# Kernel optimization log

Measured on AMD Instinct MI355X. Metric: run time of the kernel, lower is better.

## Reference

```python
import jax, jax.numpy as jnp
import numpy as np

B, N, E = 64, 512, 262144
D_EMB = 128   # 2 * embedding_dim
D_H = 128     # residue_emb_dim == iegmn_lay_hid_dim
L = 5         # iegmn_n_lays
X_INIT = 0.25 # residual mix toward original coords (IEGMN x_connection_init)


def silu(x):
    return x * jax.nn.sigmoid(x)


def _edges(k):
    # within-graph random edges: pick a graph, then a node inside it
    g = jax.random.randint(k, (E,), 0, B)
    n = jax.random.randint(jax.random.fold_in(k, 1), (E,), 0, N)
    return (g * N + n).astype(jnp.int32)


def setup_inputs() -> dict:
    key = jax.random.key(0)
    ks = jax.random.split(key, 16)
    Nt = B * N
    s = 0.05
    feat = jax.random.normal(ks[0], (Nt, D_EMB), jnp.float32)
    coords = jax.random.normal(ks[1], (Nt, 3), jnp.float32)
    c_valid = (jax.random.uniform(ks[2], (B, N)) > 0.3).astype(jnp.float32)
    c_valid = c_valid.at[:, 0].set(1.0)  # avoid empty graphs
    return {
        'feat': feat,
        'coords': coords,
        'c_valid': c_valid,
        'edge_src': _edges(ks[3]), 'edge_dst': _edges(ks[4]),
        'cross_src': _edges(ks[5]), 'cross_dst': _edges(ks[6]),
        'W_emb': jax.random.normal(ks[7], (D_H, D_EMB), jnp.float32) * s,
        'We1': jax.random.normal(ks[8], (L, 2 * D_H + 1, D_H), jnp.float32) * s,
        'be1': jnp.zeros((L, D_H), jnp.float32),
        'We2': jax.random.normal(ks[9], (L, D_H, D_H), jnp.float32) * s,
        'be2': jnp.zeros((L, D_H), jnp.float32),
        'Wx': jax.random.normal(ks[10], (L, D_H, 1), jnp.float32) * s,
        'Wh': jax.random.normal(ks[11], (L, 3 * D_H, D_H), jnp.float32) * s,
        'bh': jnp.zeros((L, D_H), jnp.float32),
        'Wfc': jax.random.normal(ks[12], (3, D_H, D_H), jnp.float32) * s,
        'bfc': jnp.zeros((3, D_H), jnp.float32),
        'Wout': jax.random.normal(ks[13], (D_H, 1), jnp.float32) * s,
        'bout': jnp.zeros((1,), jnp.float32),
    }


def _deg_inv(dst, n):
    deg = jax.ops.segment_sum(jnp.ones(dst.shape[0], jnp.float32), dst, num_segments=n)
    return (1.0 / jnp.maximum(deg, 1.0))[:, None]


def _iegmn_layer(p, src, dst, x, h, x0, h0, deg_inv):
    We1, be1, We2, be2, Wx, Wh, bh = p
    n = x.shape[0]
    dx = x[src] - x[dst]                                  # [E, 3]
    d2 = jnp.sum(dx * dx, -1, keepdims=True)              # [E, 1]
    m = silu(jnp.concatenate([h[src], h[dst], d2], -1) @ We1 + be1)
    m = silu(m @ We2 + be2)                               # [E, D_H]
    coef = jnp.tanh(m @ Wx)                               # [E, 1]
    agg_x = jax.ops.segment_sum(dx * coef, dst, num_segments=n) * deg_inv
    x_new = X_INIT * x0 + (1.0 - X_INIT) * x + agg_x
    agg_m = jax.ops.segment_sum(m, dst, num_segments=n) * deg_inv
    h_new = silu(jnp.concatenate([h, agg_m, h0], -1) @ Wh + bh)
    return x_new, h_new


def reference(feat, coords, c_valid, edge_src, edge_dst, cross_src, cross_dst,
              W_emb, We1, be1, We2, be2, Wx, Wh, bh, Wfc, bfc, Wout, bout):
    Nt = feat.shape[0]
    h = feat @ W_emb.T          # embede (no bias)
    h0, x0, x = h, coords, coords
    dgi = _deg_inv(edge_dst, Nt)
    dci = _deg_inv(cross_dst, Nt)
    for k in range(L):
        p = tuple(t[k] for t in (We1, be1, We2, be2, Wx, Wh, bh))
        # branch == 'both': run layer on graph then cross_graph with same input h
        x, c1 = _iegmn_layer(p, edge_src, edge_dst, x, h, x0, h0, dgi)
        x, c2 = _iegmn_layer(p, cross_src, cross_dst, x, h, x0, h0, dci)
        h = c2 - c1             # dropout is identity at inference
    # masked sum-pool / count
    hb = h.reshape(B, N, D_H)
    pooled = jnp.sum(hb * c_valid[..., None], axis=1) / jnp.sum(c_valid, axis=1, keepdims=True)
    z = pooled
    for i in range(Wfc.shape[0]):
        z = jax.nn.relu(z @ Wfc[i] + bfc[i])
    out = jax.nn.sigmoid(z @ Wout + bout)
    return out.reshape(-1)      # [B]
```

## Files before the change

### kernel.cpp

```cpp
#include <hip/hip_runtime.h>

#define DEVINL __device__ __forceinline__

constexpr int NT   = 32768;
constexpr int DH   = 128;
constexpr int NE   = 262144;
constexpr int BGR  = 64;
constexpr int NPG  = 512;
constexpr int LAYS = 5;

typedef __attribute__((ext_vector_type(8))) short bf16x8;
typedef __attribute__((ext_vector_type(4))) float f32x4;
typedef __attribute__((ext_vector_type(4))) unsigned int uint4v;
typedef unsigned int uint;

DEVINL float siluf(float v){ return v * (1.0f/(1.0f + __expf(-v))); }

DEVINL uint bf16_rne(float f){
  uint x = __float_as_uint(f);
  return (x + 0x7fffu + ((x>>16)&1u)) >> 16;
}

DEVINL void split8(const float* m, bf16x8& h, bf16x8& l){
  #pragma unroll
  for (int j=0;j<8;j++){
    uint x  = __float_as_uint(m[j]);
    uint hb = x >> 16;
    float hf = __uint_as_float(hb<<16);
    uint lb = bf16_rne(m[j] - hf);
    h[j] = (short)hb; l[j] = (short)lb;
  }
}

DEVINL f32x4 mma3(const uint* __restrict__ w, int i0, int i1,
                  bf16x8 ah, bf16x8 al, f32x4 acc){
  uint4v u0 = *(const uint4v*)(w + i0);
  uint4v u1 = *(const uint4v*)(w + i1);
  bf16x8 bh, bl;
  #pragma unroll
  for (int j=0;j<4;j++){
    bh[j]   = (short)(u0[j]>>16); bl[j]   = (short)(u0[j]&0xffffu);
    bh[j+4] = (short)(u1[j]>>16); bl[j+4] = (short)(u1[j]&0xffffu);
  }
  acc = __builtin_amdgcn_mfma_f32_16x16x32_bf16(al, bh, acc, 0,0,0);
  acc = __builtin_amdgcn_mfma_f32_16x16x32_bf16(ah, bl, acc, 0,0,0);
  acc = __builtin_amdgcn_mfma_f32_16x16x32_bf16(ah, bh, acc, 0,0,0);
  return acc;
}

template<int TRANS>
__global__ __launch_bounds__(256) void k_prep(const float* __restrict__ src, uint* __restrict__ dst){
  const int idx = blockIdx.x*256 + threadIdx.x;
  const int k = idx>>7, col = idx&127;
  const float v = TRANS ? src[(size_t)col*128 + k] : src[(size_t)k*128 + col];
  uint hb = __float_as_uint(v) >> 16;
  float hf = __uint_as_float(hb<<16);
  uint lb = bf16_rne(v - hf);
  const int kc = k>>5, kin = k&31, s = kin>>2;
  dst[kc*4096 + col*32 + (((s ^ (col&7)))<<2) + (kin&3)] = (hb<<16) | lb;
}

__global__ __launch_bounds__(256) void k_hist(const int* __restrict__ dst, int* __restrict__ cnt){
  int e = blockIdx.x*256 + threadIdx.x;
  atomicAdd(&cnt[dst[e]], 1);
}

__global__ __launch_bounds__(1024) void k_scan(const int* __restrict__ cnt, int* __restrict__ cur){
  __shared__ int part[1024];
  const int tid = threadIdx.x;
  const int base = tid*32;
  int s = 0;
  for (int i=0;i<32;i++) s += cnt[base+i];
  const int own = s;
  part[tid] = s; __syncthreads();
  for (int off=1; off<1024; off<<=1){
    int v = (tid>=off) ? part[tid-off] : 0;
    __syncthreads();
    part[tid] += v;
    __syncthreads();
  }
  int run = part[tid] - own;
  for (int i=0;i<32;i++){ cur[base+i] = run; run += cnt[base+i]; }
}

__global__ __launch_bounds__(256) void k_invdeg(const int* __restrict__ cnt, float* __restrict__ dinv){
  int n = blockIdx.x*256 + threadIdx.x;
  int c = cnt[n];
  dinv[n] = 1.0f / (float)(c > 1 ? c : 1);
}

__global__ __launch_bounds__(256) void k_scatter(const int* __restrict__ dst, int* __restrict__ cur,
                                                 int* __restrict__ perm){
  int e = blockIdx.x*256 + threadIdx.x;
  int p = atomicAdd(&cur[dst[e]], 1);
  perm[p] = e;
}

template<int MODE>
__global__ __launch_bounds__(512) void k_ngemm(
    const float* __restrict__ A0, const float* __restrict__ A1, const float* __restrict__ A2,
    const float* __restrict__ dinv, const uint* __restrict__ W0, const uint* __restrict__ W1,
    const float* __restrict__ bias, const float* __restrict__ c1in,
    float* __restrict__ out0, float* __restrict__ out1)
{
  __shared__ __align__(16) uint wbuf[8192];
  const int tid = threadIdx.x;
  const int wv = tid>>6, lane = tid&63, c = lane&15, q = lane>>4;
  const int row = blockIdx.x*128 + wv*16 + c;
  float dv = 1.0f;
  if constexpr (MODE>=2) dv = dinv[row];
  f32x4 accA[8], accB[8];
  #pragma unroll
  for (int t=0;t<8;t++){
    #pragma unroll
    for (int r=0;r<4;r++){ accA[t][r]=0.f; if constexpr (MODE==1) accB[t][r]=0.f; }
  }
  const int swz0 = (((2*q)  ^(c&7))<<2);
  const int swz1 = (((2*q+1)^(c&7))<<2);
  constexpr int NST = (MODE==1) ? 4 : ((MODE>=2) ? 6 : 2);
  for (int st=0; st<NST; ++st){
    __syncthreads();
    if constexpr (MODE==1){
      #pragma unroll
      for (int i=0;i<2;i++){
        ((uint4v*)wbuf)[tid + i*512]        = ((const uint4v*)(W0 + st*4096))[tid + i*512];
        ((uint4v*)(wbuf+4096))[tid + i*512] = ((const uint4v*)(W1 + st*4096))[tid + i*512];
      }
    } else {
      #pragma unroll
      for (int i=0;i<4;i++)
        ((uint4v*)wbuf)[tid + i*512] = ((const uint4v*)(W0 + st*8192))[tid + i*512];
    }
    __syncthreads();
    if constexpr (MODE==1){
      const int kb = st*32 + q*8;
      float4 v0 = *(const float4*)(A0 + (size_t)row*128 + kb);
      float4 v1 = *(const float4*)(A0 + (size_t)row*128 + kb + 4);
      float m[8] = {v0.x,v0.y,v0.z,v0.w,v1.x,v1.y,v1.z,v1.w};
      bf16x8 ah, al; split8(m, ah, al);
      #pragma unroll
      for (int t=0;t<8;t++){
        const int base = t*512 + c*32;
        accA[t] = mma3(wbuf,      base+swz0, base+swz1, ah, al, accA[t]);
        accB[t] = mma3(wbuf+4096, base+swz0, base+swz1, ah, al, accB[t]);
      }
    } else {
      #pragma unroll
      for (int ks=0; ks<2; ++ks){
        const int kc = st*2 + ks;
        const float* asrc = A0; float sc = 1.0f;
        if constexpr (MODE>=2){
          if (kc >= 8)      { asrc = A2; }
          else if (kc >= 4) { asrc = A1; sc = dv; }
        }
        const int koff = (kc&3)*32 + q*8;
        float4 v0 = *(const float4*)(asrc + (size_t)row*128 + koff);
        float4 v1 = *(const float4*)(asrc + (size_t)row*128 + koff + 4);
        float m[8] = {v0.x*sc,v0.y*sc,v0.z*sc,v0.w*sc,v1.x*sc,v1.y*sc,v1.z*sc,v1.w*sc};
        bf16x8 ah, al; split8(m, ah, al);
        #pragma unroll
        for (int t=0;t<8;t++){
          const int base = ks*4096 + t*512 + c*32;
          accA[t] = mma3(wbuf, base+swz0, base+swz1, ah, al, accA[t]);
        }
      }
    }
  }
  #pragma unroll
  for (int t=0;t<8;t++){
    const int col = t*16 + c;
    float b0 = 0.f;
    if constexpr (MODE!=0) b0 = bias[col];
    #pragma unroll
    for (int r=0;r<4;r++){
      const size_t orow = (size_t)blockIdx.x*128 + wv*16 + q*4 + r;
      float v = accA[t][r];
      if constexpr (MODE==0){
        out0[orow*128 + col] = v; out1[orow*128 + col] = v;
      } else if constexpr (MODE==1){
        out0[orow*128 + col] = v + b0;
        out1[orow*128 + col] = accB[t][r];
      } else if constexpr (MODE==2){
        out0[orow*128 + col] = siluf(v + b0);
      } else {
        out0[orow*128 + col] = siluf(v + b0) - c1in[orow*128 + col];
      }
    }
  }
}

__global__ __launch_bounds__(512) void k_edge(
    const int* __restrict__ perm, const int* __restrict__ esrc, const int* __restrict__ edst,
    const float* __restrict__ x,  const float* __restrict__ Aw, const float* __restrict__ Bw,
    const uint* __restrict__ w2p, const float* __restrict__ We1_l,
    const float* __restrict__ be2_l, const float* __restrict__ Wx_l,
    float* __restrict__ aggm, float* __restrict__ aggx)
{
  __shared__ __align__(16) uint  w2t[8192];
  __shared__ __align__(16) float w256s[128];
  __shared__ __align__(16) float wxs[128];
  __shared__ __align__(16) float be2s[128];
  __shared__ float dxs[128][3];
  __shared__ int   dsts[128];
  const int tid = threadIdx.x;
  const int wv = tid>>6, lane = tid&63, c = lane&15, q = lane>>4;
  if (tid < 128){ w256s[tid]=We1_l[256*128+tid]; wxs[tid]=Wx_l[tid]; be2s[tid]=be2_l[tid]; }
  const int er = wv*16 + c;
  const int eg = perm[blockIdx.x*128 + er];
  const int s  = esrc[eg], d = edst[eg];
  const float dx0 = x[s*3+0]-x[d*3+0];
  const float dx1 = x[s*3+1]-x[d*3+1];
  const float dx2 = x[s*3+2]-x[d*3+2];
  const float d2  = dx0*dx0 + dx1*dx1 + dx2*dx2;
  if (lane < 16){ dxs[er][0]=dx0; dxs[er][1]=dx1; dxs[er][2]=dx2; dsts[er]=d; }
  f32x4 acc[8];
  #pragma unroll
  for (int t=0;t<8;t++){ acc[t][0]=0.f; acc[t][1]=0.f; acc[t][2]=0.f; acc[t][3]=0.f; }
  const int swz0 = (((2*q)  ^(c&7))<<2);
  const int swz1 = (((2*q+1)^(c&7))<<2);
  const float* ap = Aw + (size_t)s*128;
  const float* bp = Bw + (size_t)d*128;
  for (int half=0; half<2; ++half){
    __syncthreads();
    #pragma unroll
    for (int i=0;i<4;i++)
      ((uint4v*)w2t)[tid + i*512] = ((const uint4v*)(w2p + half*8192))[tid + i*512];
    __syncthreads();
    #pragma unroll
    for (int ks=0; ks<2; ++ks){
      const int kb = half*64 + ks*32 + q*8;
      float4 av0 = *(const float4*)(ap+kb), av1 = *(const float4*)(ap+kb+4);
      float4 bv0 = *(const float4*)(bp+kb), bv1 = *(const float4*)(bp+kb+4);
      float4 w0  = *(const float4*)&w256s[kb], w1 = *(const float4*)&w256s[kb+4];
      float m[8];
      m[0]=siluf(av0.x+bv0.x+d2*w0.x); m[1]=siluf(av0.y+bv0.y+d2*w0.y);
      m[2]=siluf(av0.z+bv0.z+d2*w0.z); m[3]=siluf(av0.w+bv0.w+d2*w0.w);
      m[4]=siluf(av1.x+bv1.x+d2*w1.x); m[5]=siluf(av1.y+bv1.y+d2*w1.y);
      m[6]=siluf(av1.z+bv1.z+d2*w1.z); m[7]=siluf(av1.w+bv1.w+d2*w1.w);
      bf16x8 ah, al; split8(m, ah, al);
      #pragma unroll
      for (int t=0;t<8;t++){
        const int base = ks*4096 + t*512 + c*32;
        acc[t] = mma3(w2t, base+swz0, base+swz1, ah, al, acc[t]);
      }
    }
  }
  float pd[4];
  #pragma unroll
  for (int t=0;t<8;t++){
    const float be = be2s[t*16+c], wx = wxs[t*16+c];
    #pragma unroll
    for (int r=0;r<4;r++){
      float v = siluf(acc[t][r] + be);
      acc[t][r] = v;
      if (t==0) pd[r] = v*wx; else pd[r] += v*wx;
    }
  }
  #pragma unroll
  for (int msk=1; msk<16; msk<<=1){
    #pragma unroll
    for (int r=0;r<4;r++) pd[r] += __shfl_xor(pd[r], msk);
  }
  float coef[4];
  #pragma unroll
  for (int r=0;r<4;r++) coef[r] = tanhf(pd[r]);
  const int r0 = wv*16 + q*4;
  {
    int i = 0;
    while (i < 4){
      const int dd = dsts[r0+i];
      float sv[8];
      #pragma unroll
      for (int t=0;t<8;t++) sv[t] = acc[t][i];
      int i2 = i+1;
      while (i2 < 4 && dsts[r0+i2] == dd){
        #pragma unroll
        for (int t=0;t<8;t++) sv[t] += acc[t][i2];
        ++i2;
      }
      float* bm = aggm + (size_t)dd*128 + c;
      #pragma unroll
      for (int t=0;t<8;t++) unsafeAtomicAdd(bm + t*16, sv[t]);
      i = i2;
    }
  }
  if (c < 3){
    int i = 0;
    while (i < 4){
      const int dd = dsts[r0+i];
      float sv = dxs[r0+i][c]*coef[i];
      int i2 = i+1;
      while (i2 < 4 && dsts[r0+i2] == dd){ sv += dxs[r0+i2][c]*coef[i2]; ++i2; }
      unsafeAtomicAdd(aggx + (size_t)dd*3 + c, sv);
      i = i2;
    }
  }
}

__global__ __launch_bounds__(256) void k_xupd(float* __restrict__ x, const float* __restrict__ x0,
                                              const float* __restrict__ aggx,
                                              const float* __restrict__ dinv){
  int i = blockIdx.x*256 + threadIdx.x;
  if (i < NT*3){
    int n = i/3;
    x[i] = 0.25f*x0[i] + 0.75f*x[i] + aggx[i]*dinv[n];
  }
}

__global__ __launch_bounds__(128) void k_pool(const float* __restrict__ h,
                                              const float* __restrict__ cvalid,
                                              float* __restrict__ pooled){
  const int b = blockIdx.x, j = threadIdx.x;
  float s = 0.f, cf = 0.f;
  for (int n=0;n<NPG;n++){
    const float m = cvalid[b*NPG + n];
    s  += h[((size_t)b*NPG + n)*DH + j] * m;
    cf += m;
  }
  pooled[b*DH + j] = s / cf;
}

__global__ __launch_bounds__(256) void k_mlp(const float* __restrict__ pooled,
                                             const float* __restrict__ Wfc,
                                             const float* __restrict__ bfc,
                                             const float* __restrict__ Wout,
                                             const float* __restrict__ bout,
                                             float* __restrict__ out)
{
  __shared__ __align__(16) float z[64*132];
  __shared__ __align__(16) float wB[128*128];
  const int t = threadIdx.x;
  {
    const int n = t>>2, qq = t&3;
    const float4* p = (const float4*)(pooled + n*DH + qq*32);
    float4* w = (float4*)&z[n*132 + qq*32];
    #pragma unroll
    for (int u=0;u<8;u++) w[u] = p[u];
  }
  const int g = t>>5, lane = t&31, c0 = lane*4;
  for (int l=0;l<3;l++){
    #pragma unroll
    for (int i=0;i<16;i++){
      const int idx = t + i*256;
      ((float4*)wB)[idx] = ((const float4*)(Wfc + (size_t)l*DH*DH))[idx];
    }
    __syncthreads();
    float acc[8][4];
    #pragma unroll
    for (int i=0;i<8;i++){ acc[i][0]=0.f; acc[i][1]=0.f; acc[i][2]=0.f; acc[i][3]=0.f; }
    #pragma unroll 4
    for (int kk=0; kk<128; kk+=4){
      float4 b0=*(const float4*)&wB[(kk+0)*128+c0];
      float4 b1=*(const float4*)&wB[(kk+1)*128+c0];
      float4 b2=*(const float4*)&wB[(kk+2)*128+c0];
      float4 b3=*(const float4*)&wB[(kk+3)*128+c0];
      #pragma unroll
      for (int i=0;i<8;i++){
        float4 a=*(const float4*)&z[(g*8+i)*132 + kk];
        acc[i][0]+=a.x*b0.x+a.y*b1.x+a.z*b2.x+a.w*b3.x;
        acc[i][1]+=a.x*b0.y+a.y*b1.y+a.z*b2.y+a.w*b3.y;
        acc[i][2]+=a.x*b0.z+a.y*b1.z+a.z*b2.z+a.w*b3.z;
        acc[i][3]+=a.x*b0.w+a.y*b1.w+a.z*b2.w+a.w*b3.w;
      }
    }
    __syncthreads();
    #pragma unroll
    for (int i=0;i<8;i++){
      float v0=acc[i][0]+bfc[l*DH+c0+0]; v0 = v0>0.f?v0:0.f;
      float v1=acc[i][1]+bfc[l*DH+c0+1]; v1 = v1>0.f?v1:0.f;
      float v2=acc[i][2]+bfc[l*DH+c0+2]; v2 = v2>0.f?v2:0.f;
      float v3=acc[i][3]+bfc[l*DH+c0+3]; v3 = v3>0.f?v3:0.f;
      float4 v; v.x=v0; v.y=v1; v.z=v2; v.w=v3;
      *(float4*)&z[(g*8+i)*132 + c0] = v;
    }
    __syncthreads();
  }
  if (t < 64){
    float a = 0.f;
    for (int k2=0;k2<128;k2++) a += z[t*132 + k2]*Wout[k2];
    out[t] = 1.0f/(1.0f + __expf(-(a + bout[0])));
  }
}

extern "C" void kernel_launch(void* const* d_in, const int* in_sizes, int n_in,
                              void* d_out, int out_size, void* d_ws, size_t ws_size,
                              hipStream_t stream)
{
  (void)in_sizes; (void)n_in; (void)out_size; (void)ws_size;
  const float* feat   = (const float*)d_in[0];
  const float* coords = (const float*)d_in[1];
  const float* cvalid = (const float*)d_in[2];
  const int*   esrc   = (const int*)d_in[3];
  const int*   edst   = (const int*)d_in[4];
  const int*   csrc   = (const int*)d_in[5];
  const int*   cdst   = (const int*)d_in[6];
  const float* W_emb  = (const float*)d_in[7];
  const float* We1    = (const float*)d_in[8];
  const float* be1    = (const float*)d_in[9];
  const float* We2    = (const float*)d_in[10];
  const float* be2    = (const float*)d_in[11];
  const float* Wx     = (const float*)d_in[12];
  const float* Wh     = (const float*)d_in[13];
  const float* bh     = (const float*)d_in[14];
  const float* Wfc    = (const float*)d_in[15];
  const float* bfc    = (const float*)d_in[16];
  const float* Wout   = (const float*)d_in[17];
  const float* bout   = (const float*)d_in[18];

  float* ws = (float*)d_ws;
  float* h      = ws; ws += (size_t)NT*DH;
  float* h0     = ws; ws += (size_t)NT*DH;
  float* c1     = ws; ws += (size_t)NT*DH;
  float* Aw     = ws; ws += (size_t)NT*DH;
  float* Bw     = ws; ws += (size_t)NT*DH;
  float* aggm   = ws; ws += (size_t)NT*DH;
  float* x      = ws; ws += (size_t)NT*3;
  float* aggx   = ws; ws += (size_t)NT*3;
  float* dgi    = ws; ws += NT;
  float* dci    = ws; ws += NT;
  float* pooled = ws; ws += BGR*DH;
  int* permG  = (int*)ws; ws += NE;
  int* permC  = (int*)ws; ws += NE;
  int* cnt    = (int*)ws; ws += NT;
  int* cursor = (int*)ws; ws += NT;
  uint* pst    = (uint*)ws;
  uint* wemb_p = pst;
  const size_t LSTR = 16384*3 + 49152;
  uint* lay_p  = pst + 16384;

  k_prep<1><<<64, 256, 0, stream>>>(W_emb, wemb_p);
  for (int k=0;k<LAYS;k++){
    uint* p = lay_p + (size_t)k*LSTR;
    k_prep<0><<<64,  256, 0, stream>>>(We1 + (size_t)k*257*DH,            p);
    k_prep<0><<<64,  256, 0, stream>>>(We1 + (size_t)k*257*DH + 128*DH,   p + 16384);
    k_prep<0><<<64,  256, 0, stream>>>(We2 + (size_t)k*DH*DH,             p + 32768);
    k_prep<0><<<192, 256, 0, stream>>>(Wh  + (size_t)k*3*DH*DH,           p + 49152);
  }

  hipMemsetAsync(cnt, 0, NT*sizeof(int), stream);
  k_hist   <<<NE/256, 256, 0, stream>>>(edst, cnt);
  k_scan   <<<1, 1024, 0, stream>>>(cnt, cursor);
  k_invdeg <<<NT/256, 256, 0, stream>>>(cnt, dgi);
  k_scatter<<<NE/256, 256, 0, stream>>>(edst, cursor, permG);
  hipMemsetAsync(cnt, 0, NT*sizeof(int), stream);
  k_hist   <<<NE/256, 256, 0, stream>>>(cdst, cnt);
  k_scan   <<<1, 1024, 0, stream>>>(cnt, cursor);
  k_invdeg <<<NT/256, 256, 0, stream>>>(cnt, dci);
  k_scatter<<<NE/256, 256, 0, stream>>>(cdst, cursor, permC);

  k_ngemm<0><<<NT/128, 512, 0, stream>>>(feat, nullptr, nullptr, nullptr,
                                         wemb_p, nullptr, nullptr, nullptr, h, h0);
  hipMemcpyAsync(x, coords, (size_t)NT*3*sizeof(float), hipMemcpyDeviceToDevice, stream);

  for (int k=0; k<LAYS; k++){
    uint* p = lay_p + (size_t)k*LSTR;
    const float* We1_l = We1 + (size_t)k*257*DH;
    const float* be1_l = be1 + (size_t)k*DH;
    const float* be2_l = be2 + (size_t)k*DH;
    const float* Wx_l  = Wx  + (size_t)k*DH;
    const float* bh_l  = bh  + (size_t)k*DH;

    k_ngemm<1><<<NT/128, 512, 0, stream>>>(h, nullptr, nullptr, nullptr,
                                           p, p + 16384, be1_l, nullptr, Aw, Bw);
    hipMemsetAsync(aggm, 0, (size_t)NT*DH*sizeof(float), stream);
    hipMemsetAsync(aggx, 0, (size_t)NT*3*sizeof(float), stream);
    k_edge<<<NE/128, 512, 0, stream>>>(permG, esrc, edst, x, Aw, Bw,
                                       p + 32768, We1_l, be2_l, Wx_l, aggm, aggx);
    k_xupd<<<(NT*3+255)/256, 256, 0, stream>>>(x, coords, aggx, dgi);
    k_ngemm<2><<<NT/128, 512, 0, stream>>>(h, aggm, h0, dgi,
                                           p + 49152, nullptr, bh_l, nullptr, c1, nullptr);
    hipMemsetAsync(aggm, 0, (size_t)NT*DH*sizeof(float), stream);
    hipMemsetAsync(aggx, 0, (size_t)NT*3*sizeof(float), stream);
    k_edge<<<NE/128, 512, 0, stream>>>(permC, csrc, cdst, x, Aw, Bw,
                                       p + 32768, We1_l, be2_l, Wx_l, aggm, aggx);
    k_xupd<<<(NT*3+255)/256, 256, 0, stream>>>(x, coords, aggx, dci);
    k_ngemm<3><<<NT/128, 512, 0, stream>>>(h, aggm, h0, dci,
                                           p + 49152, nullptr, bh_l, c1, h, nullptr);
  }

  k_pool<<<BGR, 128, 0, stream>>>(h, cvalid, pooled);
  k_mlp <<<1, 256, 0, stream>>>(pooled, Wfc, bfc, Wout, bout, (float*)d_out);
}
```

Measured before the change: 1.875 ms.

## Pre-split bf16 weight layout, fuse agg zeroing into consumers, fast tanh, parallel pool

Stores weights pre-split into separate hi/lo bf16 planes so MFMA B operands load directly from LDS without per-use unpacking. Removes the per-layer memsets by zeroing aggm inside the node GEMM after it reads it and aggx inside the x update. Also swaps tanhf for an exp-based approximation and spreads the pooling reduction over 512 threads. The in-kernel zeroing adds extra global writes, and the fast tanh may overflow or lose accuracy for large inputs.

```diff
diff --git a/kernel.cpp b/kernel.cpp
--- a/kernel.cpp
+++ b/kernel.cpp
@@ -15,6 +15,7 @@
 typedef unsigned int uint;
 
 DEVINL float siluf(float v){ return v * (1.0f/(1.0f + __expf(-v))); }
+DEVINL float tanh_fast(float x){ float e = __expf(2.0f*x); return 1.0f - 2.0f/(e + 1.0f); }
 
 DEVINL uint bf16_rne(float f){
   uint x = __float_as_uint(f);
@@ -32,16 +33,7 @@
   }
 }
 
-DEVINL f32x4 mma3(const uint* __restrict__ w, int i0, int i1,
-                  bf16x8 ah, bf16x8 al, f32x4 acc){
-  uint4v u0 = *(const uint4v*)(w + i0);
-  uint4v u1 = *(const uint4v*)(w + i1);
-  bf16x8 bh, bl;
-  #pragma unroll
-  for (int j=0;j<4;j++){
-    bh[j]   = (short)(u0[j]>>16); bl[j]   = (short)(u0[j]&0xffffu);
-    bh[j+4] = (short)(u1[j]>>16); bl[j+4] = (short)(u1[j]&0xffffu);
-  }
+DEVINL f32x4 mma3(bf16x8 ah, bf16x8 al, bf16x8 bh, bf16x8 bl, f32x4 acc){
   acc = __builtin_amdgcn_mfma_f32_16x16x32_bf16(al, bh, acc, 0,0,0);
   acc = __builtin_amdgcn_mfma_f32_16x16x32_bf16(ah, bl, acc, 0,0,0);
   acc = __builtin_amdgcn_mfma_f32_16x16x32_bf16(ah, bh, acc, 0,0,0);
@@ -49,15 +41,17 @@
 }
 
 template<int TRANS>
-__global__ __launch_bounds__(256) void k_prep(const float* __restrict__ src, uint* __restrict__ dst){
+__global__ __launch_bounds__(256) void k_prep(const float* __restrict__ src, short* __restrict__ dst){
   const int idx = blockIdx.x*256 + threadIdx.x;
   const int k = idx>>7, col = idx&127;
   const float v = TRANS ? src[(size_t)col*128 + k] : src[(size_t)k*128 + col];
   uint hb = __float_as_uint(v) >> 16;
   float hf = __uint_as_float(hb<<16);
   uint lb = bf16_rne(v - hf);
-  const int kc = k>>5, kin = k&31, s = kin>>2;
-  dst[kc*4096 + col*32 + (((s ^ (col&7)))<<2) + (kin&3)] = (hb<<16) | lb;
+  const int kc = k>>5, q = (k&31)>>3, j = k&7;
+  const size_t o = (size_t)kc*8192 + q*1024 + col*8 + j;
+  dst[o]        = (short)hb;
+  dst[o + 4096] = (short)lb;
 }
 
 __global__ __launch_bounds__(256) void k_hist(const int* __restrict__ dst, int* __restrict__ cnt){
@@ -98,12 +92,12 @@
 
 template<int MODE>
 __global__ __launch_bounds__(512) void k_ngemm(
-    const float* __restrict__ A0, const float* __restrict__ A1, const float* __restrict__ A2,
-    const float* __restrict__ dinv, const uint* __restrict__ W0, const uint* __restrict__ W1,
+    const float* __restrict__ A0, float* __restrict__ A1, const float* __restrict__ A2,
+    const float* __restrict__ dinv, const short* __restrict__ W0, const short* __restrict__ W1,
     const float* __restrict__ bias, const float* __restrict__ c1in,
     float* __restrict__ out0, float* __restrict__ out1)
 {
-  __shared__ __align__(16) uint wbuf[8192];
+  __shared__ __align__(16) short wbuf[16384];
   const int tid = threadIdx.x;
   const int wv = tid>>6, lane = tid&63, c = lane&15, q = lane>>4;
   const int row = blockIdx.x*128 + wv*16 + c;
@@ -115,21 +109,20 @@
     #pragma unroll
     for (int r=0;r<4;r++){ accA[t][r]=0.f; if constexpr (MODE==1) accB[t][r]=0.f; }
   }
-  const int swz0 = (((2*q)  ^(c&7))<<2);
-  const int swz1 = (((2*q+1)^(c&7))<<2);
+  const int fo = q*1024 + c*8;
   constexpr int NST = (MODE==1) ? 4 : ((MODE>=2) ? 6 : 2);
   for (int st=0; st<NST; ++st){
     __syncthreads();
     if constexpr (MODE==1){
       #pragma unroll
       for (int i=0;i<2;i++){
-        ((uint4v*)wbuf)[tid + i*512]        = ((const uint4v*)(W0 + st*4096))[tid + i*512];
-        ((uint4v*)(wbuf+4096))[tid + i*512] = ((const uint4v*)(W1 + st*4096))[tid + i*512];
+        ((uint4v*)wbuf)[tid + i*512]         = ((const uint4v*)(W0 + st*8192))[tid + i*512];
+        ((uint4v*)(wbuf+8192))[tid + i*512]  = ((const uint4v*)(W1 + st*8192))[tid + i*512];
       }
     } else {
       #pragma unroll
       for (int i=0;i<4;i++)
-        ((uint4v*)wbuf)[tid + i*512] = ((const uint4v*)(W0 + st*8192))[tid + i*512];
+        ((uint4v*)wbuf)[tid + i*512] = ((const uint4v*)(W0 + (size_t)st*16384))[tid + i*512];
     }
     __syncthreads();
     if constexpr (MODE==1){
@@ -140,28 +133,39 @@
       bf16x8 ah, al; split8(m, ah, al);
       #pragma unroll
       for (int t=0;t<8;t++){
-        const int base = t*512 + c*32;
-        accA[t] = mma3(wbuf,      base+swz0, base+swz1, ah, al, accA[t]);
-        accB[t] = mma3(wbuf+4096, base+swz0, base+swz1, ah, al, accB[t]);
+        bf16x8 bhA = *(const bf16x8*)&wbuf[t*128 + fo];
+        bf16x8 blA = *(const bf16x8*)&wbuf[4096 + t*128 + fo];
+        bf16x8 bhB = *(const bf16x8*)&wbuf[8192 + t*128 + fo];
+        bf16x8 blB = *(const bf16x8*)&wbuf[12288 + t*128 + fo];
+        accA[t] = mma3(ah, al, bhA, blA, accA[t]);
+        accB[t] = mma3(ah, al, bhB, blB, accB[t]);
       }
     } else {
       #pragma unroll
       for (int ks=0; ks<2; ++ks){
         const int kc = st*2 + ks;
-        const float* asrc = A0; float sc = 1.0f;
+        const float* asrc = A0; float sc = 1.0f; bool zero_a1 = false;
         if constexpr (MODE>=2){
           if (kc >= 8)      { asrc = A2; }
-          else if (kc >= 4) { asrc = A1; sc = dv; }
+          else if (kc >= 4) { asrc = A1; sc = dv; zero_a1 = true; }
         }
         const int koff = (kc&3)*32 + q*8;
         float4 v0 = *(const float4*)(asrc + (size_t)row*128 + koff);
         float4 v1 = *(const float4*)(asrc + (size_t)row*128 + koff + 4);
+        if constexpr (MODE>=2){
+          if (zero_a1){
+            float4 z; z.x=0.f; z.y=0.f; z.z=0.f; z.w=0.f;
+            *(float4*)(A1 + (size_t)row*128 + koff)     = z;
+            *(float4*)(A1 + (size_t)row*128 + koff + 4) = z;
+          }
+        }
         float m[8] = {v0.x*sc,v0.y*sc,v0.z*sc,v0.w*sc,v1.x*sc,v1.y*sc,v1.z*sc,v1.w*sc};
         bf16x8 ah, al; split8(m, ah, al);
         #pragma unroll
         for (int t=0;t<8;t++){
-          const int base = ks*4096 + t*512 + c*32;
-          accA[t] = mma3(wbuf, base+swz0, base+swz1, ah, al, accA[t]);
+          bf16x8 bh = *(const bf16x8*)&wbuf[ks*8192 + t*128 + fo];
+          bf16x8 bl = *(const bf16x8*)&wbuf[ks*8192 + 4096 + t*128 + fo];
+          accA[t] = mma3(ah, al, bh, bl, accA[t]);
         }
       }
     }
@@ -192,11 +196,11 @@
 __global__ __launch_bounds__(512) void k_edge(
     const int* __restrict__ perm, const int* __restrict__ esrc, const int* __restrict__ edst,
     const float* __restrict__ x,  const float* __restrict__ Aw, const float* __restrict__ Bw,
-    const uint* __restrict__ w2p, const float* __restrict__ We1_l,
+    const short* __restrict__ w2p, const float* __restrict__ We1_l,
     const float* __restrict__ be2_l, const float* __restrict__ Wx_l,
     float* __restrict__ aggm, float* __restrict__ aggx)
 {
-  __shared__ __align__(16) uint  w2t[8192];
+  __shared__ __align__(16) short w2t[16384];
   __shared__ __align__(16) float w256s[128];
   __shared__ __align__(16) float wxs[128];
   __shared__ __align__(16) float be2s[128];
@@ -216,15 +220,14 @@
   f32x4 acc[8];
   #pragma unroll
   for (int t=0;t<8;t++){ acc[t][0]=0.f; acc[t][1]=0.f; acc[t][2]=0.f; acc[t][3]=0.f; }
-  const int swz0 = (((2*q)  ^(c&7))<<2);
-  const int swz1 = (((2*q+1)^(c&7))<<2);
+  const int fo = q*1024 + c*8;
   const float* ap = Aw + (size_t)s*128;
   const float* bp = Bw + (size_t)d*128;
   for (int half=0; half<2; ++half){
     __syncthreads();
     #pragma unroll
     for (int i=0;i<4;i++)
-      ((uint4v*)w2t)[tid + i*512] = ((const uint4v*)(w2p + half*8192))[tid + i*512];
+      ((uint4v*)w2t)[tid + i*512] = ((const uint4v*)(w2p + half*16384))[tid + i*512];
     __syncthreads();
     #pragma unroll
     for (int ks=0; ks<2; ++ks){
@@ -240,8 +243,9 @@
       bf16x8 ah, al; split8(m, ah, al);
       #pragma unroll
       for (int t=0;t<8;t++){
-        const int base = ks*4096 + t*512 + c*32;
-        acc[t] = mma3(w2t, base+swz0, base+swz1, ah, al, acc[t]);
+        bf16x8 bh = *(const bf16x8*)&w2t[ks*8192 + t*128 + fo];
+        bf16x8 bl = *(const bf16x8*)&w2t[ks*8192 + 4096 + t*128 + fo];
+        acc[t] = mma3(ah, al, bh, bl, acc[t]);
       }
     }
   }
@@ -263,7 +267,7 @@
   }
   float coef[4];
   #pragma unroll
-  for (int r=0;r<4;r++) coef[r] = tanhf(pd[r]);
+  for (int r=0;r<4;r++) coef[r] = tanh_fast(pd[r]);
   const int r0 = wv*16 + q*4;
   {
     int i = 0;
@@ -298,26 +302,36 @@
 }
 
 __global__ __launch_bounds__(256) void k_xupd(float* __restrict__ x, const float* __restrict__ x0,
-                                              const float* __restrict__ aggx,
+                                              float* __restrict__ aggx,
                                               const float* __restrict__ dinv){
   int i = blockIdx.x*256 + threadIdx.x;
   if (i < NT*3){
     int n = i/3;
     x[i] = 0.25f*x0[i] + 0.75f*x[i] + aggx[i]*dinv[n];
-  }
-}
-
-__global__ __launch_bounds__(128) void k_pool(const float* __restrict__ h,
+    aggx[i] = 0.f;
+  }
+}
+
+__global__ __launch_bounds__(512) void k_pool(const float* __restrict__ h,
                                               const float* __restrict__ cvalid,
                                               float* __restrict__ pooled){
-  const int b = blockIdx.x, j = threadIdx.x;
+  __shared__ float red[4][128];
+  __shared__ float redc[4];
+  const int b = blockIdx.x, t = threadIdx.x, j = t&127, sl = t>>7;
   float s = 0.f, cf = 0.f;
-  for (int n=0;n<NPG;n++){
+  for (int n=sl; n<NPG; n+=4){
     const float m = cvalid[b*NPG + n];
     s  += h[((size_t)b*NPG + n)*DH + j] * m;
     cf += m;
   }
-  pooled[b*DH + j] = s / cf;
+  red[sl][j] = s;
+  if (j==0) redc[sl] = cf;
+  __syncthreads();
+  if (t < 128){
+    float ss = red[0][t]+red[1][t]+red[2][t]+red[3][t];
+    float cc = redc[0]+redc[1]+redc[2]+redc[3];
+    pooled[b*DH + t] = ss / cc;
+  }
 }
 
 __global__ __launch_bounds__(256) void k_mlp(const float* __restrict__ pooled,
@@ -423,18 +437,21 @@
   int* permC  = (int*)ws; ws += NE;
   int* cnt    = (int*)ws; ws += NT;
   int* cursor = (int*)ws; ws += NT;
-  uint* pst    = (uint*)ws;
-  uint* wemb_p = pst;
-  const size_t LSTR = 16384*3 + 49152;
-  uint* lay_p  = pst + 16384;
+  short* pst    = (short*)ws;
+  short* wemb_p = pst;
+  const size_t LSTR = 32768*3 + 98304;
+  short* lay_p  = pst + 32768;
+
+  hipMemsetAsync(aggm, 0, (size_t)NT*DH*sizeof(float), stream);
+  hipMemsetAsync(aggx, 0, (size_t)NT*3*sizeof(float), stream);
 
   k_prep<1><<<64, 256, 0, stream>>>(W_emb, wemb_p);
   for (int k=0;k<LAYS;k++){
-    uint* p = lay_p + (size_t)k*LSTR;
-    k_prep<0><<<64,  256, 0, stream>>>(We1 + (size_t)k*257*DH,            p);
-    k_prep<0><<<64,  256, 0, stream>>>(We1 + (size_t)k*257*DH + 128*DH,   p + 16384);
-    k_prep<0><<<64,  256, 0, stream>>>(We2 + (size_t)k*DH*DH,             p + 32768);
-    k_prep<0><<<192, 256, 0, stream>>>(Wh  + (size_t)k*3*DH*DH,           p + 49152);
+    short* p = lay_p + (size_t)k*LSTR;
+    k_prep<0><<<64,  256, 0, stream>>>(We1 + (size_t)k*257*DH,          p);
+    k_prep<0><<<64,  256, 0, stream>>>(We1 + (size_t)k*257*DH + 128*DH, p + 32768);
+    k_prep<0><<<64,  256, 0, stream>>>(We2 + (size_t)k*DH*DH,           p + 65536);
+    k_prep<0><<<192, 256, 0, stream>>>(Wh  + (size_t)k*3*DH*DH,         p + 98304);
   }
 
   hipMemsetAsync(cnt, 0, NT*sizeof(int), stream);
@@ -453,7 +470,7 @@
   hipMemcpyAsync(x, coords, (size_t)NT*3*sizeof(float), hipMemcpyDeviceToDevice, stream);
 
   for (int k=0; k<LAYS; k++){
-    uint* p = lay_p + (size_t)k*LSTR;
+    short* p = lay_p + (size_t)k*LSTR;
     const float* We1_l = We1 + (size_t)k*257*DH;
     const float* be1_l = be1 + (size_t)k*DH;
     const float* be2_l = be2 + (size_t)k*DH;
@@ -461,23 +478,19 @@
     const float* bh_l  = bh  + (size_t)k*DH;
 
     k_ngemm<1><<<NT/128, 512, 0, stream>>>(h, nullptr, nullptr, nullptr,
-                                           p, p + 16384, be1_l, nullptr, Aw, Bw);
-    hipMemsetAsync(aggm, 0, (size_t)NT*DH*sizeof(float), stream);
-    hipMemsetAsync(aggx, 0, (size_t)NT*3*sizeof(float), stream);
+                                           p, p + 32768, be1_l, nullptr, Aw, Bw);
     k_edge<<<NE/128, 512, 0, stream>>>(permG, esrc, edst, x, Aw, Bw,
-                                       p + 32768, We1_l, be2_l, Wx_l, aggm, aggx);
+                                       p + 65536, We1_l, be2_l, Wx_l, aggm, aggx);
     k_xupd<<<(NT*3+255)/256, 256, 0, stream>>>(x, coords, aggx, dgi);
     k_ngemm<2><<<NT/128, 512, 0, stream>>>(h, aggm, h0, dgi,
-                                           p + 49152, nullptr, bh_l, nullptr, c1, nullptr);
-    hipMemsetAsync(aggm, 0, (size_t)NT*DH*sizeof(float), stream);
-    hipMemsetAsync(aggx, 0, (size_t)NT*3*sizeof(float), stream);
+                                           p + 98304, nullptr, bh_l, nullptr, c1, nullptr);
     k_edge<<<NE/128, 512, 0, stream>>>(permC, csrc, cdst, x, Aw, Bw,
-                                       p + 32768, We1_l, be2_l, Wx_l, aggm, aggx);
+                                       p + 65536, We1_l, be2_l, Wx_l, aggm, aggx);
     k_xupd<<<(NT*3+255)/256, 256, 0, stream>>>(x, coords, aggx, dci);
     k_ngemm<3><<<NT/128, 512, 0, stream>>>(h, aggm, h0, dci,
-                                           p + 49152, nullptr, bh_l, c1, h, nullptr);
-  }
-
-  k_pool<<<BGR, 128, 0, stream>>>(h, cvalid, pooled);
+                                           p + 98304, nullptr, bh_l, c1, h, nullptr);
+  }
+
+  k_pool<<<BGR, 512, 0, stream>>>(h, cvalid, pooled);
   k_mlp <<<1, 256, 0, stream>>>(pooled, Wfc, bfc, Wout, bout, (float*)d_out);
 }
```

Result: faster. 1.744 ms (-7.0%).
